# Kernel tuning notes

Measured on AMD Instinct MI355X. Metric: run time of the kernel, lower is better.

Reference implementation:

```python
import jax, jax.numpy as jnp
import numpy as np

NS = 100000; NT = 100000; M = 512; D = 256; DL = 128; H = 4; C = 256; K = 64
ITERS = 50; POS_MARGIN = 0.1


def conv1(w, b, x):
    # 1x1 Conv1d: x (B, Cin, N), w (Cout, Cin)
    return jnp.einsum('oi,bin->bon', w, x) + b[None, :, None]


def attn_block(p, x, src):
    # attentional propagation: MHA message + MLP([x, msg]) (residual added by caller)
    wq, bq, wk, bk, wv, bv, wm, bm, w1, b1, w2, b2 = p
    B, Dm, N = x.shape
    Dh = Dm // H
    Nm = src.shape[2]
    q = conv1(wq, bq, x).reshape(B, H, Dh, N)
    k = conv1(wk, bk, src).reshape(B, H, Dh, Nm)
    v = conv1(wv, bv, src).reshape(B, H, Dh, Nm)
    a = jax.nn.softmax(jnp.einsum('bhdn,bhdm->bhnm', q, k) * (1.0 / np.sqrt(Dh)), axis=-1)
    msg = jnp.einsum('bhnm,bhdm->bhdn', a, v).reshape(B, Dm, N)
    msg = conv1(wm, bm, msg)
    h = jax.nn.relu(conv1(w1, b1, jnp.concatenate([x, msg], axis=1)))
    return conv1(w2, b2, h)


def nn_id(points, nodes):
    # 1-NN node id per point; points (N,3), nodes (M,3)
    d = (jnp.sum(points * points, 1, keepdims=True) - 2.0 * points @ nodes.T
         + jnp.sum(nodes * nodes, 1)[None, :])
    return jnp.argmin(d, axis=1)


def build_patches(pcd_id, m, k):
    # grouping_wrapper: first k point indices assigned to each node, -1 padded
    n = pcd_id.shape[0]
    order = jnp.argsort(pcd_id)  # stable
    sid = pcd_id[order]
    starts = jnp.searchsorted(sid, jnp.arange(m))
    rank = jnp.arange(n) - starts[sid]
    patch = jnp.full((m, k), -1, jnp.int32)
    patch = patch.at[sid, rank].set(order.astype(jnp.int32), mode='drop')  # rank>=k dropped
    mask = (patch < 0).astype(jnp.float32)
    return jnp.where(patch < 0, 0, patch), mask


def log_optimal_transport(scores, alpha, iters):
    b, m, n = scores.shape
    bins0 = jnp.full((b, m, 1), alpha)
    bins1 = jnp.full((b, 1, n), alpha)
    corner = jnp.full((b, 1, 1), alpha)
    Z = jnp.concatenate([jnp.concatenate([scores, bins0], 2),
                         jnp.concatenate([bins1, corner], 2)], 1)
    norm = -np.log(m + n)
    log_mu = jnp.concatenate([jnp.full((m,), norm, jnp.float32), jnp.array([np.log(n) + norm], jnp.float32)])
    log_nu = jnp.concatenate([jnp.full((n,), norm, jnp.float32), jnp.array([np.log(m) + norm], jnp.float32)])
    log_mu = jnp.broadcast_to(log_mu, (b, m + 1))
    log_nu = jnp.broadcast_to(log_nu, (b, n + 1))

    def body(carry, _):
        u, v = carry
        u = log_mu - jax.nn.logsumexp(Z + v[:, None, :], axis=2)
        v = log_nu - jax.nn.logsumexp(Z + u[:, :, None], axis=1)
        return (u, v), None

    (u, v), _ = jax.lax.scan(body, (jnp.zeros((b, m + 1)), jnp.zeros((b, n + 1))), None, length=iters)
    return Z + u[:, :, None] + v[:, None, :] - norm


def rpmnet_sinkhorn(log_alpha, bins0, bins1, iters):
    b = log_alpha.shape[0]
    corner = jnp.zeros((b, 1, 1), log_alpha.dtype)
    la = jnp.concatenate([jnp.concatenate([log_alpha, bins0], 2),
                          jnp.concatenate([bins1, corner], 2)], 1)

    def body(la, _):
        row = la - jax.nn.logsumexp(la, axis=2, keepdims=True)
        la = jnp.concatenate([row[:, :-1, :], la[:, -1:, :]], axis=1)  # normalize all rows but slack
        col = la - jax.nn.logsumexp(la, axis=1, keepdims=True)
        la = jnp.concatenate([col[:, :, :-1], la[:, :, -1:]], axis=2)  # normalize all cols but slack
        return la, None

    la, _ = jax.lax.scan(body, la, None, length=iters)
    return la


def _forward(src_pcd_c, tgt_pcd_c, src_node_c, tgt_node_c, src_feats_c, tgt_feats_c,
             src_final_f, tgt_final_f, rot, trans, src_pcd_raw, tgt_pcd_raw,
             c_wq, c_bq, c_wk, c_bk, c_wv, c_bv, c_wm, c_bm, c_w1, c_b1, c_w2, c_b2,
             l_wq, l_bq, l_wk, l_bk, l_wv, l_bv, l_wm, l_bm, l_w1, l_b1, l_w2, l_b2,
             fp_w, fp_b, lfp_w, lfp_b, bin_score, node_corr):
    # KNN assignment + patch grouping (irregular gather/scatter)
    src_patch, src_mask = build_patches(nn_id(src_pcd_c, src_node_c), M, K)
    tgt_patch, tgt_mask = build_patches(nn_id(tgt_pcd_c, tgt_node_c), M, K)
    # coarse attention stack (self, cross, self) with residuals
    cp = lambda i: (c_wq[i], c_bq[i], c_wk[i], c_bk[i], c_wv[i], c_bv[i], c_wm[i], c_bm[i],
                    c_w1[i], c_b1[i], c_w2[i], c_b2[i])
    sf, tf = src_feats_c, tgt_feats_c
    sf = sf + attn_block(cp(0), sf, sf); tf = tf + attn_block(cp(0), tf, tf)
    sf = sf + attn_block(cp(1), sf, tf); tf = tf + attn_block(cp(1), tf, sf)  # sequential, like torch
    sf = sf + attn_block(cp(2), sf, sf); tf = tf + attn_block(cp(2), tf, tf)
    sf = conv1(fp_w, fp_b, sf); tf = conv1(fp_w, fp_b, tf)
    scores = jnp.einsum('bdn,bdm->bnm', sf, tf) / np.sqrt(D)
    scores = log_optimal_transport(scores, bin_score, ITERS)
    # correspondence-driven patch gather
    sn = node_corr[:, 0]; tn = node_corr[:, 1]
    src_sel = src_patch[sn].reshape(-1)
    tgt_sel = tgt_patch[tn].reshape(-1)
    smask = src_mask[sn]; tmask = tgt_mask[tn]  # (C,K)
    # GT local scores (training path)
    src_raw_t = (rot @ src_pcd_raw.T + trans).T
    sc = src_raw_t[src_sel].reshape(C, K, 3)
    tc = tgt_pcd_raw[tgt_sel].reshape(C, K, 3)
    d2 = jnp.maximum(jnp.sum(sc * sc, -1)[:, :, None] + jnp.sum(tc * tc, -1)[:, None, :]
                     - 2.0 * jnp.einsum('cnd,cmd->cnm', sc, tc), 0.0)
    gt = (jnp.sqrt(d2) < POS_MARGIN).astype(jnp.float32)
    row = jnp.maximum(1.0 - jnp.sum(gt, -1), 0.0)[:, :, None]
    col = jnp.maximum(1.0 - jnp.sum(gt, -2), 0.0)[:, None, :]
    col = jnp.concatenate([col, jnp.zeros((C, 1, 1), jnp.float32)], -1)
    gt = jnp.concatenate([jnp.concatenate([gt, row], -1), col], -2)  # (C,K+1,K+1)
    gt = gt.at[:, :-1, :].multiply(1.0 - smask[:, :, None])
    gt = gt.at[:, :, :-1].multiply(1.0 - tmask[:, None, :])
    # local patch features + attention stack
    spf = src_final_f[src_sel].reshape(C, K, DL).transpose(0, 2, 1)  # (C,DL,K)
    tpf = tgt_final_f[tgt_sel].reshape(C, K, DL).transpose(0, 2, 1)
    lp = lambda i: (l_wq[i], l_bq[i], l_wk[i], l_bk[i], l_wv[i], l_bv[i], l_wm[i], l_bm[i],
                    l_w1[i], l_b1[i], l_w2[i], l_b2[i])
    spf = spf + attn_block(lp(0), spf, spf); tpf = tpf + attn_block(lp(0), tpf, tpf)
    spf = spf + attn_block(lp(1), spf, tpf); tpf = tpf + attn_block(lp(1), tpf, spf)
    spf = spf + attn_block(lp(2), spf, spf); tpf = tpf + attn_block(lp(2), tpf, tpf)
    spf = conv1(lfp_w, lfp_b, spf); tpf = conv1(lfp_w, lfp_b, tpf)
    ls = jnp.einsum('bdn,bdm->bnm', spf, tpf) / np.sqrt(DL)
    ls = jnp.where(smask[:, :, None] > 0, -1e6, ls)
    ls = jnp.where(tmask[:, None, :] > 0, -1e6, ls)
    ls = rpmnet_sinkhorn(ls, jnp.zeros((C, K, 1), jnp.float32), jnp.zeros((C, 1, K), jnp.float32), ITERS)
    return scores, ls, gt


def setup_inputs() -> dict:
    key = jax.random.key(0)
    ks = jax.random.split(key, 48)

    def rn(i, shape, scale):
        return jax.random.normal(ks[i], shape, jnp.float32) * scale

    inp = {}
    inp['src_pcd_c'] = jax.random.uniform(ks[0], (NS, 3), jnp.float32)
    inp['tgt_pcd_c'] = jax.random.uniform(ks[1], (NT, 3), jnp.float32)
    inp['src_node_c'] = jax.random.uniform(ks[2], (M, 3), jnp.float32)
    inp['tgt_node_c'] = jax.random.uniform(ks[3], (M, 3), jnp.float32)
    inp['src_feats_c'] = rn(4, (1, D, M), 1.0)
    inp['tgt_feats_c'] = rn(5, (1, D, M), 1.0)
    inp['src_final_f'] = rn(6, (NS, DL), 1.0)
    inp['tgt_final_f'] = rn(7, (NT, DL), 1.0)
    inp['rot'] = jnp.eye(3, dtype=jnp.float32)
    inp['trans'] = jnp.zeros((3, 1), jnp.float32)
    inp['src_pcd_raw'] = jax.random.uniform(ks[8], (NS, 3), jnp.float32)
    inp['tgt_pcd_raw'] = jax.random.uniform(ks[9], (NT, 3), jnp.float32)
    inp['node_corr'] = jax.random.randint(ks[10], (C, 2), 0, M)
    i = 11
    for pre, d in (('c_', D), ('l_', DL)):
        for nm in ('wq', 'wk', 'wv', 'wm'):
            inp[pre + nm] = rn(i, (3, d, d), 1.0 / np.sqrt(d)); i += 1
            inp[pre + 'b' + nm[1]] = jnp.zeros((3, d), jnp.float32)
        inp[pre + 'w1'] = rn(i, (3, 2 * d, 2 * d), 1.0 / np.sqrt(2 * d)); i += 1
        inp[pre + 'b1'] = jnp.zeros((3, 2 * d), jnp.float32)
        inp[pre + 'w2'] = rn(i, (3, d, 2 * d), 1.0 / np.sqrt(2 * d)); i += 1
        inp[pre + 'b2'] = jnp.zeros((3, d), jnp.float32)
    inp['fp_w'] = rn(i, (D, D), 1.0 / np.sqrt(D)); i += 1
    inp['fp_b'] = jnp.zeros((D,), jnp.float32)
    inp['lfp_w'] = rn(i, (DL, DL), 1.0 / np.sqrt(DL)); i += 1
    inp['lfp_b'] = jnp.zeros((DL,), jnp.float32)
    inp['bin_score'] = jnp.ones((), jnp.float32)
    return inp


def reference(src_pcd_c, tgt_pcd_c, src_node_c, tgt_node_c, src_feats_c, tgt_feats_c,
              src_final_f, tgt_final_f, rot, trans, src_pcd_raw, tgt_pcd_raw,
              c_wq, c_bq, c_wk, c_bk, c_wv, c_bv, c_wm, c_bm, c_w1, c_b1, c_w2, c_b2,
              l_wq, l_bq, l_wk, l_bk, l_wv, l_bv, l_wm, l_bm, l_w1, l_b1, l_w2, l_b2,
              fp_w, fp_b, lfp_w, lfp_b, bin_score, node_corr):
    return _forward(src_pcd_c, tgt_pcd_c, src_node_c, tgt_node_c, src_feats_c, tgt_feats_c,
                    src_final_f, tgt_final_f, rot, trans, src_pcd_raw, tgt_pcd_raw,
                    c_wq, c_bq, c_wk, c_bk, c_wv, c_bv, c_wm, c_bm, c_w1, c_b1, c_w2, c_b2,
                    l_wq, l_bq, l_wk, l_bk, l_wv, l_bv, l_wm, l_bm, l_w1, l_b1, l_w2, l_b2,
                    fp_w, fp_b, lfp_w, lfp_b, bin_score, node_corr)
```

## Files before the change

kernel.cpp:

```cpp
#include <hip/hip_runtime.h>
#include <math.h>

static constexpr int NODES = 512;
static constexpr int CC    = 256;
static constexpr int KP    = 64;
static constexpr int ZDIM  = 513;
static constexpr int TPNB  = 16;
static constexpr int TPROWS = 33;

typedef unsigned short u16;
typedef short bf16x8 __attribute__((ext_vector_type(8)));
typedef float f32x4 __attribute__((ext_vector_type(4)));

__device__ __forceinline__ u16 f2b(float f){
  unsigned u = __float_as_uint(f);
  unsigned r = (u + 0x7FFF + ((u >> 16) & 1)) >> 16;
  return (u16)r;
}
__device__ __forceinline__ float b2f(u16 h){ return __uint_as_float(((unsigned)h) << 16); }
__device__ __forceinline__ f32x4 mfma16(bf16x8 a, bf16x8 b, f32x4 c){
  return __builtin_amdgcn_mfma_f32_16x16x32_bf16(a, b, c, 0, 0, 0);
}
__device__ __forceinline__ void astore(float* p, float v){
  __hip_atomic_store(p, v, __ATOMIC_RELAXED, __HIP_MEMORY_SCOPE_AGENT);
// ... 151 lines not shown
  __syncthreads();
  if (i >= n) return;
  int m = lid[t];
  int r = hist[(long)bb*NODES + m];
  for (int q = 0; q < t; ++q) r += (lid[q] == m) ? 1 : 0;
  if (r < KP) patch[m*KP + r] = i;
}

__global__ __launch_bounds__(256) void coarse_qkv(
    const u16* __restrict__ cf, int cross, int side0,
    const u16* __restrict__ Wq, const u16* __restrict__ Wk, const u16* __restrict__ Wv,
    const float* __restrict__ bq, const float* __restrict__ bk, const float* __restrict__ bv,
    u16* __restrict__ qb, u16* __restrict__ kb, u16* __restrict__ vtb)
{
  int z = blockIdx.x;
  int side = side0 + z/24, rem = z%24, proj = rem >> 3, slice = rem & 7;
  const u16* x = cf + (long)side*131072;
  const u16* s = cross ? cf + (long)(1-side)*131072 : x;
  const u16* in = (proj == 0) ? x : s;
  const u16* W  = (proj==0)?Wq:(proj==1)?Wk:Wv;
  const float* bi = (proj==0)?bq:(proj==1)?bk:bv;
  int n0 = slice << 6;
  int wv_ = threadIdx.x >> 6, L = threadIdx.x & 63, lr = L & 15, lk = L >> 4;
  const u16* inb = in + (long)(n0 + lr)*256 + 8*lk;
  for (int oi = 0; oi < 4; ++oi){
    int o0 = (wv_*4 + oi) << 4;
    const u16* wrow = W + (long)(o0 + lr)*256 + 8*lk;
    f32x4 acc[4] = {};
#pragma unroll
    for (int ks = 0; ks < 8; ++ks){
      bf16x8 b = *(const bf16x8*)(wrow + ks*32);
#pragma unroll
      for (int a = 0; a < 4; ++a){
        bf16x8 av = *(const bf16x8*)(inb + a*16*256 + ks*32);
        acc[a] = mfma16(av, b, acc[a]);
      }
    }
    int col = o0 + lr;
    float bvv = bi[col];
    if (proj < 2){
      u16* o = (proj==0 ? qb : kb) + ((long)side*512 + n0)*256 + col;
#pragma unroll
      for (int a = 0; a < 4; ++a)
#pragma unroll
        for (int q_ = 0; q_ < 4; ++q_)
          o[(long)(a*16 + lk*4 + q_)*256] = f2b(acc[a][q_] + bvv);
    } else {
      u16* o = vtb + ((long)side*256 + col)*512 + n0;
#pragma unroll
      for (int a = 0; a < 4; ++a)
#pragma unroll
        for (int q_ = 0; q_ < 4; ++q_)
          o[a*16 + lk*4 + q_] = f2b(acc[a][q_] + bvv);
    }
  }
}

__global__ __launch_bounds__(256) void coarse_attn(
    const u16* __restrict__ qb, const u16* __restrict__ kb,
    const u16* __restrict__ vtb, u16* __restrict__ msgb, int side0)
{
  __shared__ u16 P[64][512];
  __shared__ float rmx[64][4], rsm[64][4];
  int z = blockIdx.x;
  int side = side0 + (z >> 5); int rem = z & 31;
  int head = rem >> 3, qs = rem & 7;
  int wv_ = threadIdx.x >> 6, L = threadIdx.x & 63, lr = L & 15, lk = L >> 4;
  const u16* q = qb + ((long)side*512 + qs*64)*256 + head*64;
  const u16* k = kb + (long)side*512*256 + head*64;
  const u16* vt = vtb + ((long)side*256 + head*64)*512;

  bf16x8 af[4][2];
#pragma unroll
  for (int a = 0; a < 4; ++a)
#pragma unroll
    for (int ks = 0; ks < 2; ++ks)
      af[a][ks] = *(const bf16x8*)(q + (long)(a*16 + lr)*256 + ks*32 + 8*lk);

  f32x4 sc[4][8] = {};
  for (int b = 0; b < 8; ++b){
    const u16* krow = k + (long)(wv_*128 + b*16 + lr)*256 + 8*lk;
#pragma unroll
    for (int ks = 0; ks < 2; ++ks){
      bf16x8 bf = *(const bf16x8*)(krow + ks*32);
#pragma unroll
      for (int a = 0; a < 4; ++a)
        sc[a][b] = mfma16(af[a][ks], bf, sc[a][b]);
    }
  }
  const float SC = 0.125f;
#pragma unroll
  for (int a = 0; a < 4; ++a)
#pragma unroll
    for (int q_ = 0; q_ < 4; ++q_){
      float m = sc[a][0][q_];
#pragma unroll
      for (int b = 1; b < 8; ++b) m = fmaxf(m, sc[a][b][q_]);
      m = fmaxf(m, __shfl_xor(m, 1)); m = fmaxf(m, __shfl_xor(m, 2));
      m = fmaxf(m, __shfl_xor(m, 4)); m = fmaxf(m, __shfl_xor(m, 8));
      if (lr == 0) rmx[a*16 + lk*4 + q_][wv_] = m;
    }
  __syncthreads();
#pragma unroll
  for (int a = 0; a < 4; ++a)
#pragma unroll
    for (int q_ = 0; q_ < 4; ++q_){
      int row = a*16 + lk*4 + q_;
      float m = fmaxf(fmaxf(rmx[row][0], rmx[row][1]), fmaxf(rmx[row][2], rmx[row][3]));
      float s = 0.f;
#pragma unroll
      for (int b = 0; b < 8; ++b){
        float e = __expf((sc[a][b][q_] - m)*SC);
        sc[a][b][q_] = e; s += e;
      }
      s += __shfl_xor(s,1); s += __shfl_xor(s,2); s += __shfl_xor(s,4); s += __shfl_xor(s,8);
      if (lr == 0) rsm[row][wv_] = s;
    }
  __syncthreads();
#pragma unroll
  for (int a = 0; a < 4; ++a)
#pragma unroll
    for (int q_ = 0; q_ < 4; ++q_){
      int row = a*16 + lk*4 + q_;
      float inv = 1.f / (rsm[row][0]+rsm[row][1]+rsm[row][2]+rsm[row][3]);
#pragma unroll
      for (int b = 0; b < 8; ++b)
        P[row][wv_*128 + b*16 + lr] = f2b(sc[a][b][q_] * inv);
    }
  __syncthreads();
  f32x4 mv[4] = {};
  for (int ks = 0; ks < 16; ++ks){
    bf16x8 bf = *(const bf16x8*)(vt + (long)(wv_*16 + lr)*512 + ks*32 + 8*lk);
#pragma unroll
    for (int a = 0; a < 4; ++a){
      bf16x8 av = *(const bf16x8*)(&P[a*16 + lr][ks*32 + 8*lk]);
      mv[a] = mfma16(av, bf, mv[a]);
    }
  }
  u16* o = msgb + ((long)side*512 + qs*64)*256 + head*64 + wv_*16 + lr;
#pragma unroll
  for (int a = 0; a < 4; ++a)
#pragma unroll
    for (int q_ = 0; q_ < 4; ++q_)
      o[(long)(a*16 + lk*4 + q_)*256] = f2b(mv[a][q_]);
}

__global__ __launch_bounds__(512) void coarse_ffn(
    const u16* __restrict__ msgb, u16* __restrict__ cf, float* __restrict__ cff,
    const u16* __restrict__ Wm, const float* __restrict__ bm,
    const u16* __restrict__ W1, const float* __restrict__ b1,
    const u16* __restrict__ W2, const float* __restrict__ b2, int side0)
{
  __shared__ u16 m2[64*256];
  __shared__ u16 h1[64*512];
  int z = blockIdx.x;
  int side = side0 + (z >> 3), slice = z & 7;
  int wv_ = threadIdx.x >> 6, L = threadIdx.x & 63, lr = L & 15, lk = L >> 4;
  const u16* msg = msgb + ((long)side*512 + slice*64)*256;
  u16* x = cf + ((long)side*512 + slice*64)*256;
  float* xf = cff + ((long)side*512 + slice*64)*256;
  for (int oi = 0; oi < 2; ++oi){
    int o0 = (wv_*2 + oi) << 4;
    f32x4 acc[4] = {};
    const u16* wrow = Wm + (long)(o0+lr)*256 + 8*lk;
#pragma unroll
    for (int ks = 0; ks < 8; ++ks){
      bf16x8 b = *(const bf16x8*)(wrow + ks*32);
#pragma unroll
      for (int a = 0; a < 4; ++a){
        bf16x8 av = *(const bf16x8*)(msg + (long)(a*16+lr)*256 + ks*32 + 8*lk);
        acc[a] = mfma16(av, b, acc[a]);
      }
    }
    int col = o0 + lr; float bb = bm[col];
#pragma unroll
    for (int a = 0; a < 4; ++a)
#pragma unroll
      for (int q_ = 0; q_ < 4; ++q_)
        m2[(a*16+lk*4+q_)*256 + col] = f2b(acc[a][q_] + bb);
  }
  __syncthreads();
  for (int oi = 0; oi < 4; ++oi){
    int o0 = (wv_*4 + oi) << 4;
    f32x4 acc[4] = {};
    const u16* wrow = W1 + (long)(o0+lr)*512 + 8*lk;
#pragma unroll
    for (int ks = 0; ks < 16; ++ks){
      int kk = ks*32;
      bf16x8 b = *(const bf16x8*)(wrow + kk);
#pragma unroll
      for (int a = 0; a < 4; ++a){
        bf16x8 av;
        if (kk < 256) av = *(const bf16x8*)(x + (long)(a*16+lr)*256 + kk + 8*lk);
        else          av = *(const bf16x8*)(&m2[(a*16+lr)*256 + kk - 256 + 8*lk]);
        acc[a] = mfma16(av, b, acc[a]);
      }
    }
    int col = o0 + lr; float bb = b1[col];
#pragma unroll
    for (int a = 0; a < 4; ++a)
#pragma unroll
      for (int q_ = 0; q_ < 4; ++q_)
        h1[(a*16+lk*4+q_)*512 + col] = f2b(fmaxf(acc[a][q_] + bb, 0.f));
  }
  __syncthreads();
  for (int oi = 0; oi < 2; ++oi){
    int o0 = (wv_*2 + oi) << 4;
    f32x4 acc[4] = {};
    const u16* wrow = W2 + (long)(o0+lr)*512 + 8*lk;
#pragma unroll
    for (int ks = 0; ks < 16; ++ks){
      bf16x8 b = *(const bf16x8*)(wrow + ks*32);
#pragma unroll
      for (int a = 0; a < 4; ++a){
        bf16x8 av = *(const bf16x8*)(&h1[(a*16+lr)*512 + ks*32 + 8*lk]);
        acc[a] = mfma16(av, b, acc[a]);
      }
    }
    int col = o0 + lr; float bb = b2[col];
#pragma unroll
    for (int a = 0; a < 4; ++a)
#pragma unroll
      for (int q_ = 0; q_ < 4; ++q_){
        long idx = (long)(a*16+lk*4+q_)*256 + col;
        float v = acc[a][q_] + bb + xf[idx];
        xf[idx] = v;
        x[idx] = f2b(v);
      }
  }
}

__global__ __launch_bounds__(256) void coarse_proj(
    const u16* __restrict__ cf, const u16* __restrict__ W,
    const float* __restrict__ bias, u16* __restrict__ out)
{
  int z = blockIdx.x;
  int side = z >> 3, slice = z & 7;
  const u16* in = cf + (long)side*131072;
  u16* o = out + (long)side*131072;
  int n0 = slice << 6;
  int wv_ = threadIdx.x >> 6, L = threadIdx.x & 63, lr = L & 15, lk = L >> 4;
  const u16* inb = in + (long)(n0 + lr)*256 + 8*lk;
  for (int oi = 0; oi < 4; ++oi){
    int o0 = (wv_*4 + oi) << 4;
    const u16* wrow = W + (long)(o0 + lr)*256 + 8*lk;
    f32x4 acc[4] = {};
#pragma unroll
    for (int ks = 0; ks < 8; ++ks){
      bf16x8 b = *(const bf16x8*)(wrow + ks*32);
#pragma unroll
      for (int a = 0; a < 4; ++a){
        bf16x8 av = *(const bf16x8*)(inb + a*16*256 + ks*32);
        acc[a] = mfma16(av, b, acc[a]);
      }
    }
    int col = o0 + lr; float bb = bias[col];
#pragma unroll
    for (int a = 0; a < 4; ++a)
#pragma unroll
      for (int q_ = 0; q_ < 4; ++q_)
        o[(long)(n0 + a*16 + lk*4 + q_)*256 + col] = f2b(acc[a][q_] + bb);
  }
}

__global__ __launch_bounds__(256) void coarse_scores(
    const u16* __restrict__ sfp, const u16* __restrict__ tfp, float* __restrict__ Z)
{
  int n0 = blockIdx.y << 6, m0 = blockIdx.x << 6;
  int wv_ = threadIdx.x >> 6, L = threadIdx.x & 63, lr = L & 15, lk = L >> 4;
  f32x4 acc[4] = {};
  const u16* arow = sfp + (long)(n0 + lr)*256 + 8*lk;
  const u16* brow = tfp + (long)(m0 + wv_*16 + lr)*256 + 8*lk;
#pragma unroll
// ... 149 lines not shown
    for (int j = lane; j < 513; j += 64) orow[j] = zr[j] + uu + M[j] + outadd;
  }
}

__device__ void layerapp(
    u16* __restrict__ x, const u16* __restrict__ s, u16* __restrict__ pool,
    const u16* __restrict__ Wq, const u16* __restrict__ Wk,
    const u16* __restrict__ Wv, const u16* __restrict__ Wm,
    const u16* __restrict__ W1, const u16* __restrict__ W2,
    const float* __restrict__ bq, const float* __restrict__ bk,
    const float* __restrict__ bv, const float* __restrict__ bm,
    const float* __restrict__ b1, const float* __restrict__ b2)
{
  int tid = threadIdx.x;
  int wv8 = tid >> 6, L = tid & 63, lr = L & 15, lk = L >> 4;
  u16* qS = pool; u16* kS = pool + 8192; u16* vT = pool + 16384; u16* msgS = pool + 24576;

#pragma unroll
  for (int proj = 0; proj < 3; ++proj){
    const u16* in = proj ? s : x;
    const u16* W = proj==0?Wq:proj==1?Wk:Wv;
    const float* bi = proj==0?bq:proj==1?bk:bv;
    int o0 = wv8 << 4;
    f32x4 acc[4] = {};
    const u16* wrow = W + (long)(o0+lr)*128 + 8*lk;
    const u16* inr = in + (long)lr*128 + 8*lk;
#pragma unroll
    for (int ks = 0; ks < 4; ++ks){
      bf16x8 b = *(const bf16x8*)(wrow + ks*32);
#pragma unroll
      for (int a = 0; a < 4; ++a){
        bf16x8 av = *(const bf16x8*)(inr + a*16*128 + ks*32);
        acc[a] = mfma16(av, b, acc[a]);
      }
    }
    int col = o0 + lr; float bb = bi[col];
    if (proj < 2){
      u16* dst = (proj==0 ? qS : kS);
#pragma unroll
      for (int a = 0; a < 4; ++a)
#pragma unroll
        for (int q_ = 0; q_ < 4; ++q_)
          dst[(a*16 + lk*4 + q_)*128 + col] = f2b(acc[a][q_] + bb);
    } else {
#pragma unroll
      for (int a = 0; a < 4; ++a)
#pragma unroll
        for (int q_ = 0; q_ < 4; ++q_)
          vT[col*64 + a*16 + lk*4 + q_] = f2b(acc[a][q_] + bb);
    }
  }
  __syncthreads();
  int h = wv8 >> 1, half = wv8 & 1;
  bf16x8 qf[2], kf[4];
#pragma unroll
  for (int ai = 0; ai < 2; ++ai){
    int a = half*2 + ai;
    qf[ai] = *(const bf16x8*)(&qS[(a*16+lr)*128 + h*32 + 8*lk]);
  }
#pragma unroll
  for (int b = 0; b < 4; ++b)
    kf[b] = *(const bf16x8*)(&kS[(b*16+lr)*128 + h*32 + 8*lk]);
  f32x4 sc[2][4] = {};
#pragma unroll
  for (int b = 0; b < 4; ++b)
#pragma unroll
    for (int ai = 0; ai < 2; ++ai)
      sc[ai][b] = mfma16(qf[ai], kf[b], sc[ai][b]);
  const float SCs = 0.17677669529663687f;
  float invs[2][4];
#pragma unroll
  for (int ai = 0; ai < 2; ++ai)
#pragma unroll
    for (int q_ = 0; q_ < 4; ++q_){
      float m = sc[ai][0][q_];
#pragma unroll
      for (int b = 1; b < 4; ++b) m = fmaxf(m, sc[ai][b][q_]);
// ... 2 lines not shown
      float ss = 0.f;
#pragma unroll
      for (int b = 0; b < 4; ++b){
        float e = __expf((sc[ai][b][q_] - m)*SCs);
        sc[ai][b][q_] = e; ss += e;
      }
      ss += __shfl_xor(ss,1); ss += __shfl_xor(ss,2); ss += __shfl_xor(ss,4); ss += __shfl_xor(ss,8);
      invs[ai][q_] = 1.f/ss;
    }
  __syncthreads();
  u16* P = pool + h*4096;
#pragma unroll
  for (int ai = 0; ai < 2; ++ai){
    int a = half*2 + ai;
#pragma unroll
    for (int q_ = 0; q_ < 4; ++q_)
#pragma unroll
      for (int b = 0; b < 4; ++b)
        P[(a*16 + lk*4 + q_)*64 + b*16 + lr] = f2b(sc[ai][b][q_] * invs[ai][q_]);
  }
  f32x4 mv[2][2] = {};
#pragma unroll
  for (int ks = 0; ks < 2; ++ks)
#pragma unroll
    for (int bt = 0; bt < 2; ++bt){
      bf16x8 bf = *(const bf16x8*)(&vT[(h*32 + bt*16 + lr)*64 + ks*32 + 8*lk]);
#pragma unroll
      for (int ai = 0; ai < 2; ++ai){
        int a = half*2 + ai;
        bf16x8 av = *(const bf16x8*)(&P[(a*16+lr)*64 + ks*32 + 8*lk]);
        mv[ai][bt] = mfma16(av, bf, mv[ai][bt]);
      }
    }
#pragma unroll
  for (int ai = 0; ai < 2; ++ai){
    int a = half*2 + ai;
#pragma unroll
    for (int bt = 0; bt < 2; ++bt)
#pragma unroll
      for (int q_ = 0; q_ < 4; ++q_)
        msgS[(a*16 + lk*4 + q_)*128 + h*32 + bt*16 + lr] = f2b(mv[ai][bt][q_]);
  }
  __syncthreads();
  u16* m2 = pool;
  {
    int o0 = wv8 << 4;
    f32x4 acc[4] = {};
    const u16* wrow = Wm + (long)(o0+lr)*128 + 8*lk;
#pragma unroll
    for (int ks = 0; ks < 4; ++ks){
      bf16x8 b = *(const bf16x8*)(wrow + ks*32);
#pragma unroll
      for (int a = 0; a < 4; ++a){
        bf16x8 av = *(const bf16x8*)(&msgS[(a*16+lr)*128 + ks*32 + 8*lk]);
        acc[a] = mfma16(av, b, acc[a]);
      }
    }
    int col = o0+lr; float bb = bm[col];
#pragma unroll
    for (int a = 0; a < 4; ++a)
#pragma unroll
      for (int q_ = 0; q_ < 4; ++q_)
        m2[(a*16+lk*4+q_)*128 + col] = f2b(acc[a][q_] + bb);
  }
  __syncthreads();
  u16* h1 = pool + 8192;
#pragma unroll
  for (int oi = 0; oi < 2; ++oi){
    int o0 = (wv8*2 + oi) << 4;
    f32x4 acc[4] = {};
    const u16* wrow = W1 + (long)(o0+lr)*256 + 8*lk;
#pragma unroll
    for (int ks = 0; ks < 8; ++ks){
      int kk = ks*32;
      bf16x8 b = *(const bf16x8*)(wrow + kk);
#pragma unroll
      for (int a = 0; a < 4; ++a){
        bf16x8 av;
        if (kk < 128) av = *(const bf16x8*)(x + (long)(a*16+lr)*128 + kk + 8*lk);
        else          av = *(const bf16x8*)(&m2[(a*16+lr)*128 + kk - 128 + 8*lk]);
        acc[a] = mfma16(av, b, acc[a]);
      }
    }
    int col = o0+lr; float bb = b1[col];
#pragma unroll
    for (int a = 0; a < 4; ++a)
#pragma unroll
      for (int q_ = 0; q_ < 4; ++q_)
        h1[(a*16+lk*4+q_)*256 + col] = f2b(fmaxf(acc[a][q_] + bb, 0.f));
  }
  __syncthreads();
  {
    int o0 = wv8 << 4;
    f32x4 acc[4] = {};
    const u16* wrow = W2 + (long)(o0+lr)*256 + 8*lk;
#pragma unroll
    for (int ks = 0; ks < 8; ++ks){
      bf16x8 b = *(const bf16x8*)(wrow + ks*32);
#pragma unroll
      for (int a = 0; a < 4; ++a){
        bf16x8 av = *(const bf16x8*)(&h1[(a*16+lr)*256 + ks*32 + 8*lk]);
        acc[a] = mfma16(av, b, acc[a]);
      }
    }
    int col = o0+lr; float bb = b2[col];
#pragma unroll
    for (int a = 0; a < 4; ++a)
#pragma unroll
      for (int q_ = 0; q_ < 4; ++q_){
        int ri = (a*16+lk*4+q_)*128 + col;
        x[ri] = f2b(acc[a][q_] + bb + b2f(x[ri]));
      }
  }
  __syncthreads();
}

__device__ void local_role(char* arena, int c,
    const float* __restrict__ Fs, const float* __restrict__ Ft,
    const int* __restrict__ patch_s, const int* __restrict__ patch_t,
    const int* __restrict__ corr,
    const int* __restrict__ cnt_s, const int* __restrict__ cnt_t,
    const u16* WlQ, const u16* WlK, const u16* WlV, const u16* WlM,
    const u16* Wl1, const u16* Wl2, const u16* Wlfp,
    const float* lbq, const float* lbk, const float* lbv, const float* lbm,
    const float* lb1, const float* lb2, const float* lfpB,
    float* __restrict__ out_ls)
{
  u16* X    = (u16*)arena;
  u16* pool = (u16*)(arena + 32768);
  float* LA = (float*)(arena + 98304);
  float* ET = (float*)(arena + 115712);
  float* uvec = (float*)(arena + 133120);
  float* vvec = (float*)(arena + 133440);
  float* u0s  = (float*)(arena + 133760);
  float* Ul   = (float*)(arena + 134080);
  float* Vl   = (float*)(arena + 134400);
  int* sel    = (int*)(arena + 134720);
  int tid = threadIdx.x;
  int wv8 = tid >> 6, L = tid & 63, lr = L & 15, lk = L >> 4;

  if (tid < 128){
    int side = tid >> 6, n = tid & 63;
    int node = corr[c*2 + side];
    sel[tid] = (side ? patch_t : patch_s)[node*KP + n];
  }
  __syncthreads();
  for (int e = tid; e < 16384; e += 512){
    int side = e >> 13, r = e & 8191, n = r >> 7, d = r & 127;
    const float* F = side ? Ft : Fs;
    X[e] = f2b(F[(long)sel[side*64 + n]*128 + d]);
  }
  __syncthreads();

  for (int l = 0; l < 3; ++l){
// ... 18 lines not shown
    const u16* wrow = Wlfp + (long)(o0+lr)*128 + 8*lk;
    const u16* inr = in + (long)lr*128 + 8*lk;
#pragma unroll
    for (int ks = 0; ks < 4; ++ks){
      bf16x8 b = *(const bf16x8*)(wrow + ks*32);
#pragma unroll
      for (int a = 0; a < 4; ++a){
        bf16x8 av = *(const bf16x8*)(inr + a*16*128 + ks*32);
        acc[a] = mfma16(av, b, acc[a]);
      }
    }
    int col = o0 + lr; float bb = lfpB[col];
#pragma unroll
    for (int a = 0; a < 4; ++a)
#pragma unroll
      for (int q_ = 0; q_ < 4; ++q_)
        dst[(a*16 + lk*4 + q_)*128 + col] = f2b(acc[a][q_] + bb);
  }
  __syncthreads();

  int cs = cnt_s[corr[c*2]], ct = cnt_t[corr[c*2+1]];
  for (int t_ = wv8; t_ < 16; t_ += 8){
    int mt = t_ >> 2, nt = t_ & 3;
    f32x4 acc = {};
    const u16* arow = sp + (mt*16 + lr)*128 + 8*lk;
    const u16* brow = tp + (nt*16 + lr)*128 + 8*lk;
#pragma unroll
    for (int ks = 0; ks < 4; ++ks){
      bf16x8 a = *(const bf16x8*)(arow + ks*32);
      bf16x8 b = *(const bf16x8*)(brow + ks*32);
      acc = mfma16(a, b, acc);
    }
    const float SCS = 0.08838834764831845f;
#pragma unroll
    for (int q_ = 0; q_ < 4; ++q_){
      int row = mt*16 + lk*4 + q_;
      int col = nt*16 + lr;
      float v = acc[q_] * SCS;
      if (row >= cs || col >= ct) v = -1000000.0f;
      LA[row*66 + col] = v;
    }
  }
  if (tid < 65){ LA[64*66 + tid] = 0.f; LA[tid*66 + 64] = 0.f; uvec[tid] = 1.f; vvec[tid] = 1.f; }
  __syncthreads();

// ... 126 lines not shown
    const float* lbq, const float* lbk, const float* lbv, const float* lbm,
    const float* lb1, const float* lb2, const float* lfpB,
    float* out_ls,
    const float* sraw, const float* traw, const float* rot, const float* trans,
    float* out_gt)
{
  __shared__ __align__(16) char arena[ARENA];
  int b = blockIdx.x;
  if (b < 128){
    if ((b & 7) == 0)
      transport_role(arena, b >> 3, Z, Zt, Rr, Cc, UU, VV, out0, outadd);
    return;
  }
  b -= 128;
  if (b < CC)
    gt_role(arena, b, sraw, traw, rot, trans,
            patch_s, patch_t, corr, cnt_s, cnt_t, out_gt);
  else
    local_role(arena, b - CC, Fs, Ft, patch_s, patch_t, corr, cnt_s, cnt_t,
               WlQ, WlK, WlV, WlM, Wl1, Wl2, Wlfp,
               lbq, lbk, lbv, lbm, lb1, lb2, lfpB, out_ls);
}

extern "C" void kernel_launch(void* const* d_in, const int* in_sizes, int n_in,
                              void* d_out, int out_size, void* d_ws, size_t ws_size,
                              hipStream_t stream)
{
  const float* src_pcd_c  = (const float*)d_in[0];
  const float* tgt_pcd_c  = (const float*)d_in[1];
  const float* src_node_c = (const float*)d_in[2];
  const float* tgt_node_c = (const float*)d_in[3];
  const float* src_feats  = (const float*)d_in[4];
  const float* tgt_feats  = (const float*)d_in[5];
  const float* src_final  = (const float*)d_in[6];
  const float* tgt_final  = (const float*)d_in[7];
  const float* rot        = (const float*)d_in[8];
// ... 82 lines not shown
      tgt_pcd_c, NT, tgt_node_c, id_t, hist_t, nbs, nbnn,
      src_feats, tgt_feats, cf, cff);
  scan_kernel2<<<256, 256, 0, stream>>>(hist_s, nbs, cnt_s, hist_t, nbt, cnt_t);
  rank_kernel<<<nbs + nbt, 256, 0, stream>>>(
      id_s, NS, hist_s, patch_s, id_t, NT, hist_t, patch_t, nbs);

  int crossL[3] = {0, 1, 0};
  for (int l = 0; l < 3; ++l){
    u16* wq = WcQ + (size_t)l*65536; u16* wk = WcK + (size_t)l*65536;
    u16* wv = WcV + (size_t)l*65536; u16* wm = WcM + (size_t)l*65536;
    u16* w1 = Wc1 + (size_t)l*262144; u16* w2 = Wc2 + (size_t)l*131072;
    const float* bq = c_bq + (size_t)l*256; const float* bk = c_bk + (size_t)l*256;
    const float* bv = c_bv + (size_t)l*256; const float* bm = c_bm + (size_t)l*256;
    const float* b1 = c_b1 + (size_t)l*512; const float* b2 = c_b2 + (size_t)l*256;
    if (!crossL[l]){
      coarse_qkv<<<48, 256, 0, stream>>>(cf, 0, 0, wq, wk, wv, bq, bk, bv, qb, kb, vtb);
      coarse_attn<<<64, 256, 0, stream>>>(qb, kb, vtb, msgb, 0);
      coarse_ffn<<<16, 512, 0, stream>>>(msgb, cf, cff, wm, bm, w1, b1, w2, b2, 0);
    } else {
      for (int sd = 0; sd < 2; ++sd){
        coarse_qkv<<<24, 256, 0, stream>>>(cf, 1, sd, wq, wk, wv, bq, bk, bv, qb, kb, vtb);
        coarse_attn<<<32, 256, 0, stream>>>(qb, kb, vtb, msgb, sd);
        coarse_ffn<<<8, 512, 0, stream>>>(msgb, cf, cff, wm, bm, w1, b1, w2, b2, sd);
      }
    }
  }
  coarse_proj<<<16, 256, 0, stream>>>(cf, Wfp, fp_b, sfpb);
  coarse_scores<<<dim3(8,8), 256, 0, stream>>>(sfpb, sfpb + 131072, Zx);
  fill_border<<<3, 256, 0, stream>>>(Zx, bin_score);
  transpose_k<<<dim3(17,17), 256, 0, stream>>>(Zx, Zt, ZDIM);

  mega<<<128 + CC + CC, 512, 0, stream>>>(
      Zx, Zt, Rr, Cc, UU, VV, out0, logf(1024.0f),
      src_final, tgt_final, patch_s, patch_t, node_corr, cnt_s, cnt_t,
      WlQ, WlK, WlV, WlM, Wl1, Wl2, Wlfp,
      l_bq, l_bk, l_bv, l_bm, l_b1, l_b2, lfp_b,
      out_ls,
      src_raw, tgt_raw, rot, trans, out_gt);

  (void)n_in; (void)out_size; (void)ws_size;
}
```

Measured before the change: 971.7 us.

## Shrink coarse-layer tiles for more blocks, swizzle LDS layouts, reorder mega roles

The coarse QKV, attention, projection and FFN kernels now use smaller row tiles (32 or 16 rows instead of 64), so each launch has two to four times as many blocks and the GPU's compute units are better filled. Shared-memory tiles in the coarse and local attention paths use an XOR swizzle, plus a padded vT stride, to avoid LDS bank conflicts on MFMA operand loads. The mega kernel now puts local_role blocks before gt_role blocks so the heavier work is scheduled earlier. In exchange, weight rows are reloaded from global memory by more blocks, and each block does less MFMA work per weight load.

```diff
diff --git a/kernel.cpp b/kernel.cpp
--- a/kernel.cpp
+++ b/kernel.cpp
@@ -189,24 +189,24 @@
     u16* __restrict__ qb, u16* __restrict__ kb, u16* __restrict__ vtb)
 {
   int z = blockIdx.x;
-  int side = side0 + z/24, rem = z%24, proj = rem >> 3, slice = rem & 7;
+  int side = side0 + z/48, rem = z%48, proj = rem >> 4, slice = rem & 15;
   const u16* x = cf + (long)side*131072;
   const u16* s = cross ? cf + (long)(1-side)*131072 : x;
   const u16* in = (proj == 0) ? x : s;
   const u16* W  = (proj==0)?Wq:(proj==1)?Wk:Wv;
   const float* bi = (proj==0)?bq:(proj==1)?bk:bv;
-  int n0 = slice << 6;
+  int n0 = slice << 5;
   int wv_ = threadIdx.x >> 6, L = threadIdx.x & 63, lr = L & 15, lk = L >> 4;
   const u16* inb = in + (long)(n0 + lr)*256 + 8*lk;
   for (int oi = 0; oi < 4; ++oi){
     int o0 = (wv_*4 + oi) << 4;
     const u16* wrow = W + (long)(o0 + lr)*256 + 8*lk;
-    f32x4 acc[4] = {};
+    f32x4 acc[2] = {};
 #pragma unroll
     for (int ks = 0; ks < 8; ++ks){
       bf16x8 b = *(const bf16x8*)(wrow + ks*32);
 #pragma unroll
-      for (int a = 0; a < 4; ++a){
+      for (int a = 0; a < 2; ++a){
         bf16x8 av = *(const bf16x8*)(inb + a*16*256 + ks*32);
         acc[a] = mfma16(av, b, acc[a]);
       }
@@ -216,14 +216,14 @@
     if (proj < 2){
       u16* o = (proj==0 ? qb : kb) + ((long)side*512 + n0)*256 + col;
 #pragma unroll
-      for (int a = 0; a < 4; ++a)
+      for (int a = 0; a < 2; ++a)
 #pragma unroll
         for (int q_ = 0; q_ < 4; ++q_)
           o[(long)(a*16 + lk*4 + q_)*256] = f2b(acc[a][q_] + bvv);
     } else {
       u16* o = vtb + ((long)side*256 + col)*512 + n0;
 #pragma unroll
-      for (int a = 0; a < 4; ++a)
+      for (int a = 0; a < 2; ++a)
 #pragma unroll
         for (int q_ = 0; q_ < 4; ++q_)
           o[a*16 + lk*4 + q_] = f2b(acc[a][q_] + bvv);
@@ -235,37 +235,37 @@
     const u16* __restrict__ qb, const u16* __restrict__ kb,
     const u16* __restrict__ vtb, u16* __restrict__ msgb, int side0)
 {
-  __shared__ u16 P[64][512];
-  __shared__ float rmx[64][4], rsm[64][4];
+  __shared__ u16 P[32*512];
+  __shared__ float rmx[32][4], rsm[32][4];
   int z = blockIdx.x;
-  int side = side0 + (z >> 5); int rem = z & 31;
-  int head = rem >> 3, qs = rem & 7;
+  int side = side0 + (z >> 6); int rem = z & 63;
+  int head = rem >> 4, qs = rem & 15;
   int wv_ = threadIdx.x >> 6, L = threadIdx.x & 63, lr = L & 15, lk = L >> 4;
-  const u16* q = qb + ((long)side*512 + qs*64)*256 + head*64;
+  const u16* q = qb + ((long)side*512 + qs*32)*256 + head*64;
   const u16* k = kb + (long)side*512*256 + head*64;
   const u16* vt = vtb + ((long)side*256 + head*64)*512;
 
-  bf16x8 af[4][2];
-#pragma unroll
-  for (int a = 0; a < 4; ++a)
+  bf16x8 af[2][2];
+#pragma unroll
+  for (int a = 0; a < 2; ++a)
 #pragma unroll
     for (int ks = 0; ks < 2; ++ks)
       af[a][ks] = *(const bf16x8*)(q + (long)(a*16 + lr)*256 + ks*32 + 8*lk);
 
-  f32x4 sc[4][8] = {};
+  f32x4 sc[2][8] = {};
   for (int b = 0; b < 8; ++b){
     const u16* krow = k + (long)(wv_*128 + b*16 + lr)*256 + 8*lk;
 #pragma unroll
     for (int ks = 0; ks < 2; ++ks){
       bf16x8 bf = *(const bf16x8*)(krow + ks*32);
 #pragma unroll
-      for (int a = 0; a < 4; ++a)
+      for (int a = 0; a < 2; ++a)
         sc[a][b] = mfma16(af[a][ks], bf, sc[a][b]);
     }
   }
   const float SC = 0.125f;
 #pragma unroll
-  for (int a = 0; a < 4; ++a)
+  for (int a = 0; a < 2; ++a)
 #pragma unroll
     for (int q_ = 0; q_ < 4; ++q_){
       float m = sc[a][0][q_];
@@ -277,7 +277,7 @@
     }
   __syncthreads();
 #pragma unroll
-  for (int a = 0; a < 4; ++a)
+  for (int a = 0; a < 2; ++a)
 #pragma unroll
     for (int q_ = 0; q_ < 4; ++q_){
       int row = a*16 + lk*4 + q_;
@@ -293,115 +293,104 @@
     }
   __syncthreads();
 #pragma unroll
-  for (int a = 0; a < 4; ++a)
+  for (int a = 0; a < 2; ++a)
 #pragma unroll
     for (int q_ = 0; q_ < 4; ++q_){
       int row = a*16 + lk*4 + q_;
       float inv = 1.f / (rsm[row][0]+rsm[row][1]+rsm[row][2]+rsm[row][3]);
 #pragma unroll
       for (int b = 0; b < 8; ++b)
-        P[row][wv_*128 + b*16 + lr] = f2b(sc[a][b][q_] * inv);
-    }
-  __syncthreads();
-  f32x4 mv[4] = {};
+        P[row*512 + ((wv_*128 + b*16 + lr) ^ ((row&7)<<3))] = f2b(sc[a][b][q_] * inv);
+    }
+  __syncthreads();
+  f32x4 mv[2] = {};
   for (int ks = 0; ks < 16; ++ks){
     bf16x8 bf = *(const bf16x8*)(vt + (long)(wv_*16 + lr)*512 + ks*32 + 8*lk);
 #pragma unroll
-    for (int a = 0; a < 4; ++a){
-      bf16x8 av = *(const bf16x8*)(&P[a*16 + lr][ks*32 + 8*lk]);
+    for (int a = 0; a < 2; ++a){
+      bf16x8 av = *(const bf16x8*)(&P[(a*16 + lr)*512 + ((ks*32 + 8*lk) ^ ((lr&7)<<3))]);
       mv[a] = mfma16(av, bf, mv[a]);
     }
   }
-  u16* o = msgb + ((long)side*512 + qs*64)*256 + head*64 + wv_*16 + lr;
-#pragma unroll
-  for (int a = 0; a < 4; ++a)
+  u16* o = msgb + ((long)side*512 + qs*32)*256 + head*64 + wv_*16 + lr;
+#pragma unroll
+  for (int a = 0; a < 2; ++a)
 #pragma unroll
     for (int q_ = 0; q_ < 4; ++q_)
       o[(long)(a*16 + lk*4 + q_)*256] = f2b(mv[a][q_]);
 }
 
-__global__ __launch_bounds__(512) void coarse_ffn(
+__global__ __launch_bounds__(256) void coarse_ffn(
     const u16* __restrict__ msgb, u16* __restrict__ cf, float* __restrict__ cff,
     const u16* __restrict__ Wm, const float* __restrict__ bm,
     const u16* __restrict__ W1, const float* __restrict__ b1,
     const u16* __restrict__ W2, const float* __restrict__ b2, int side0)
 {
-  __shared__ u16 m2[64*256];
-  __shared__ u16 h1[64*512];
+  __shared__ u16 m2[16*256];
+  __shared__ u16 h1[16*512];
   int z = blockIdx.x;
-  int side = side0 + (z >> 3), slice = z & 7;
+  int side = side0 + (z >> 5), slice = z & 31;
   int wv_ = threadIdx.x >> 6, L = threadIdx.x & 63, lr = L & 15, lk = L >> 4;
-  const u16* msg = msgb + ((long)side*512 + slice*64)*256;
-  u16* x = cf + ((long)side*512 + slice*64)*256;
-  float* xf = cff + ((long)side*512 + slice*64)*256;
-  for (int oi = 0; oi < 2; ++oi){
-    int o0 = (wv_*2 + oi) << 4;
-    f32x4 acc[4] = {};
+  const u16* msg = msgb + ((long)side*512 + slice*16)*256;
+  u16* x = cf + ((long)side*512 + slice*16)*256;
+  float* xf = cff + ((long)side*512 + slice*16)*256;
+  for (int oi = 0; oi < 4; ++oi){
+    int o0 = (wv_*4 + oi) << 4;
+    f32x4 acc = {};
     const u16* wrow = Wm + (long)(o0+lr)*256 + 8*lk;
 #pragma unroll
     for (int ks = 0; ks < 8; ++ks){
       bf16x8 b = *(const bf16x8*)(wrow + ks*32);
-#pragma unroll
-      for (int a = 0; a < 4; ++a){
-        bf16x8 av = *(const bf16x8*)(msg + (long)(a*16+lr)*256 + ks*32 + 8*lk);
-        acc[a] = mfma16(av, b, acc[a]);
-      }
+      bf16x8 av = *(const bf16x8*)(msg + (long)lr*256 + ks*32 + 8*lk);
+      acc = mfma16(av, b, acc);
     }
     int col = o0 + lr; float bb = bm[col];
 #pragma unroll
-    for (int a = 0; a < 4; ++a)
-#pragma unroll
-      for (int q_ = 0; q_ < 4; ++q_)
-        m2[(a*16+lk*4+q_)*256 + col] = f2b(acc[a][q_] + bb);
-  }
-  __syncthreads();
-  for (int oi = 0; oi < 4; ++oi){
-    int o0 = (wv_*4 + oi) << 4;
-    f32x4 acc[4] = {};
+    for (int q_ = 0; q_ < 4; ++q_){
+      int row = lk*4 + q_;
+      m2[row*256 + (col ^ ((row&7)<<3))] = f2b(acc[q_] + bb);
+    }
+  }
+  __syncthreads();
+  for (int oi = 0; oi < 8; ++oi){
+    int o0 = (wv_*8 + oi) << 4;
+    f32x4 acc = {};
     const u16* wrow = W1 + (long)(o0+lr)*512 + 8*lk;
 #pragma unroll
     for (int ks = 0; ks < 16; ++ks){
       int kk = ks*32;
       bf16x8 b = *(const bf16x8*)(wrow + kk);
-#pragma unroll
-      for (int a = 0; a < 4; ++a){
-        bf16x8 av;
-        if (kk < 256) av = *(const bf16x8*)(x + (long)(a*16+lr)*256 + kk + 8*lk);
-        else          av = *(const bf16x8*)(&m2[(a*16+lr)*256 + kk - 256 + 8*lk]);
-        acc[a] = mfma16(av, b, acc[a]);
-      }
+      bf16x8 av;
+      if (kk < 256) av = *(const bf16x8*)(x + (long)lr*256 + kk + 8*lk);
+      else          av = *(const bf16x8*)(&m2[lr*256 + ((kk - 256 + 8*lk) ^ ((lr&7)<<3))]);
+      acc = mfma16(av, b, acc);
     }
     int col = o0 + lr; float bb = b1[col];
 #pragma unroll
-    for (int a = 0; a < 4; ++a)
-#pragma unroll
-      for (int q_ = 0; q_ < 4; ++q_)
-        h1[(a*16+lk*4+q_)*512 + col] = f2b(fmaxf(acc[a][q_] + bb, 0.f));
-  }
-  __syncthreads();
-  for (int oi = 0; oi < 2; ++oi){
-    int o0 = (wv_*2 + oi) << 4;
-    f32x4 acc[4] = {};
+    for (int q_ = 0; q_ < 4; ++q_){
+      int row = lk*4 + q_;
+      h1[row*512 + (col ^ ((row&7)<<3))] = f2b(fmaxf(acc[q_] + bb, 0.f));
+    }
+  }
+  __syncthreads();
+  for (int oi = 0; oi < 4; ++oi){
+    int o0 = (wv_*4 + oi) << 4;
+    f32x4 acc = {};
     const u16* wrow = W2 + (long)(o0+lr)*512 + 8*lk;
 #pragma unroll
     for (int ks = 0; ks < 16; ++ks){
       bf16x8 b = *(const bf16x8*)(wrow + ks*32);
-#pragma unroll
-      for (int a = 0; a < 4; ++a){
-        bf16x8 av = *(const bf16x8*)(&h1[(a*16+lr)*512 + ks*32 + 8*lk]);
-        acc[a] = mfma16(av, b, acc[a]);
-      }
+      bf16x8 av = *(const bf16x8*)(&h1[lr*512 + ((ks*32 + 8*lk) ^ ((lr&7)<<3))]);
+      acc = mfma16(av, b, acc);
     }
     int col = o0 + lr; float bb = b2[col];
 #pragma unroll
-    for (int a = 0; a < 4; ++a)
-#pragma unroll
-      for (int q_ = 0; q_ < 4; ++q_){
-        long idx = (long)(a*16+lk*4+q_)*256 + col;
-        float v = acc[a][q_] + bb + xf[idx];
-        xf[idx] = v;
-        x[idx] = f2b(v);
-      }
+    for (int q_ = 0; q_ < 4; ++q_){
+      long idx = (long)(lk*4+q_)*256 + col;
+      float v = acc[q_] + bb + xf[idx];
+      xf[idx] = v;
+      x[idx] = f2b(v);
+    }
   }
 }
 
@@ -410,28 +399,28 @@
     const float* __restrict__ bias, u16* __restrict__ out)
 {
   int z = blockIdx.x;
-  int side = z >> 3, slice = z & 7;
+  int side = z >> 4, slice = z & 15;
   const u16* in = cf + (long)side*131072;
   u16* o = out + (long)side*131072;
-  int n0 = slice << 6;
+  int n0 = slice << 5;
   int wv_ = threadIdx.x >> 6, L = threadIdx.x & 63, lr = L & 15, lk = L >> 4;
   const u16* inb = in + (long)(n0 + lr)*256 + 8*lk;
   for (int oi = 0; oi < 4; ++oi){
     int o0 = (wv_*4 + oi) << 4;
     const u16* wrow = W + (long)(o0 + lr)*256 + 8*lk;
-    f32x4 acc[4] = {};
+    f32x4 acc[2] = {};
 #pragma unroll
     for (int ks = 0; ks < 8; ++ks){
       bf16x8 b = *(const bf16x8*)(wrow + ks*32);
 #pragma unroll
-      for (int a = 0; a < 4; ++a){
+      for (int a = 0; a < 2; ++a){
         bf16x8 av = *(const bf16x8*)(inb + a*16*256 + ks*32);
         acc[a] = mfma16(av, b, acc[a]);
       }
     }
     int col = o0 + lr; float bb = bias[col];
 #pragma unroll
-    for (int a = 0; a < 4; ++a)
+    for (int a = 0; a < 2; ++a)
 #pragma unroll
       for (int q_ = 0; q_ < 4; ++q_)
         o[(long)(n0 + a*16 + lk*4 + q_)*256 + col] = f2b(acc[a][q_] + bb);
@@ -611,7 +600,8 @@
 {
   int tid = threadIdx.x;
   int wv8 = tid >> 6, L = tid & 63, lr = L & 15, lk = L >> 4;
-  u16* qS = pool; u16* kS = pool + 8192; u16* vT = pool + 16384; u16* msgS = pool + 24576;
+  u16* qS = pool; u16* kS = pool + 8192; u16* vT = pool + 16384; u16* msgS = pool + 24832;
+  int swr = (lr & 7) << 3;
 
 #pragma unroll
   for (int proj = 0; proj < 3; ++proj){
@@ -637,14 +627,16 @@
 #pragma unroll
       for (int a = 0; a < 4; ++a)
 #pragma unroll
+        for (int q_ = 0; q_ < 4; ++q_){
+          int row = a*16 + lk*4 + q_;
+          dst[row*128 + (col ^ ((row&7)<<3))] = f2b(acc[a][q_] + bb);
+        }
+    } else {
+#pragma unroll
+      for (int a = 0; a < 4; ++a)
+#pragma unroll
         for (int q_ = 0; q_ < 4; ++q_)
-          dst[(a*16 + lk*4 + q_)*128 + col] = f2b(acc[a][q_] + bb);
-    } else {
-#pragma unroll
-      for (int a = 0; a < 4; ++a)
-#pragma unroll
-        for (int q_ = 0; q_ < 4; ++q_)
-          vT[col*64 + a*16 + lk*4 + q_] = f2b(acc[a][q_] + bb);
+          vT[col*66 + a*16 + lk*4 + q_] = f2b(acc[a][q_] + bb);
     }
   }
   __syncthreads();
@@ -653,11 +645,11 @@
 #pragma unroll
   for (int ai = 0; ai < 2; ++ai){
     int a = half*2 + ai;
-    qf[ai] = *(const bf16x8*)(&qS[(a*16+lr)*128 + h*32 + 8*lk]);
+    qf[ai] = *(const bf16x8*)(&qS[(a*16+lr)*128 + ((h*32 + 8*lk) ^ swr)]);
   }
 #pragma unroll
   for (int b = 0; b < 4; ++b)
-    kf[b] = *(const bf16x8*)(&kS[(b*16+lr)*128 + h*32 + 8*lk]);
+    kf[b] = *(const bf16x8*)(&kS[(b*16+lr)*128 + ((h*32 + 8*lk) ^ swr)]);
   f32x4 sc[2][4] = {};
 #pragma unroll
   for (int b = 0; b < 4; ++b)
@@ -690,21 +682,23 @@
   for (int ai = 0; ai < 2; ++ai){
     int a = half*2 + ai;
 #pragma unroll
-    for (int q_ = 0; q_ < 4; ++q_)
+    for (int q_ = 0; q_ < 4; ++q_){
+      int row = a*16 + lk*4 + q_;
 #pragma unroll
       for (int b = 0; b < 4; ++b)
-        P[(a*16 + lk*4 + q_)*64 + b*16 + lr] = f2b(sc[ai][b][q_] * invs[ai][q_]);
+        P[row*64 + ((b*16 + lr) ^ ((row&7)<<3))] = f2b(sc[ai][b][q_] * invs[ai][q_]);
+    }
   }
   f32x4 mv[2][2] = {};
 #pragma unroll
   for (int ks = 0; ks < 2; ++ks)
 #pragma unroll
     for (int bt = 0; bt < 2; ++bt){
-      bf16x8 bf = *(const bf16x8*)(&vT[(h*32 + bt*16 + lr)*64 + ks*32 + 8*lk]);
+      bf16x8 bf = *(const bf16x8*)(&vT[(h*32 + bt*16 + lr)*66 + ks*32 + 8*lk]);
 #pragma unroll
       for (int ai = 0; ai < 2; ++ai){
         int a = half*2 + ai;
-        bf16x8 av = *(const bf16x8*)(&P[(a*16+lr)*64 + ks*32 + 8*lk]);
+        bf16x8 av = *(const bf16x8*)(&P[(a*16+lr)*64 + ((ks*32 + 8*lk) ^ swr)]);
         mv[ai][bt] = mfma16(av, bf, mv[ai][bt]);
       }
     }
@@ -714,8 +708,10 @@
 #pragma unroll
     for (int bt = 0; bt < 2; ++bt)
 #pragma unroll
-      for (int q_ = 0; q_ < 4; ++q_)
-        msgS[(a*16 + lk*4 + q_)*128 + h*32 + bt*16 + lr] = f2b(mv[ai][bt][q_]);
+      for (int q_ = 0; q_ < 4; ++q_){
+        int row = a*16 + lk*4 + q_;
+        msgS[row*128 + ((h*32 + bt*16 + lr) ^ ((row&7)<<3))] = f2b(mv[ai][bt][q_]);
+      }
   }
   __syncthreads();
   u16* m2 = pool;
@@ -728,7 +724,7 @@
       bf16x8 b = *(const bf16x8*)(wrow + ks*32);
 #pragma unroll
       for (int a = 0; a < 4; ++a){
-        bf16x8 av = *(const bf16x8*)(&msgS[(a*16+lr)*128 + ks*32 + 8*lk]);
+        bf16x8 av = *(const bf16x8*)(&msgS[(a*16+lr)*128 + ((ks*32 + 8*lk) ^ swr)]);
         acc[a] = mfma16(av, b, acc[a]);
       }
     }
@@ -736,8 +732,10 @@
 #pragma unroll
     for (int a = 0; a < 4; ++a)
 #pragma unroll
-      for (int q_ = 0; q_ < 4; ++q_)
-        m2[(a*16+lk*4+q_)*128 + col] = f2b(acc[a][q_] + bb);
+      for (int q_ = 0; q_ < 4; ++q_){
+        int row = a*16+lk*4+q_;
+        m2[row*128 + (col ^ ((row&7)<<3))] = f2b(acc[a][q_] + bb);
+      }
   }
   __syncthreads();
   u16* h1 = pool + 8192;
@@ -754,7 +752,7 @@
       for (int a = 0; a < 4; ++a){
         bf16x8 av;
         if (kk < 128) av = *(const bf16x8*)(x + (long)(a*16+lr)*128 + kk + 8*lk);
-        else          av = *(const bf16x8*)(&m2[(a*16+lr)*128 + kk - 128 + 8*lk]);
+        else          av = *(const bf16x8*)(&m2[(a*16+lr)*128 + ((kk - 128 + 8*lk) ^ swr)]);
         acc[a] = mfma16(av, b, acc[a]);
       }
     }
@@ -762,8 +760,10 @@
 #pragma unroll
     for (int a = 0; a < 4; ++a)
 #pragma unroll
-      for (int q_ = 0; q_ < 4; ++q_)
-        h1[(a*16+lk*4+q_)*256 + col] = f2b(fmaxf(acc[a][q_] + bb, 0.f));
+      for (int q_ = 0; q_ < 4; ++q_){
+        int row = a*16+lk*4+q_;
+        h1[row*256 + (col ^ ((row&7)<<3))] = f2b(fmaxf(acc[a][q_] + bb, 0.f));
+      }
   }
   __syncthreads();
   {
@@ -775,7 +775,7 @@
       bf16x8 b = *(const bf16x8*)(wrow + ks*32);
 #pragma unroll
       for (int a = 0; a < 4; ++a){
-        bf16x8 av = *(const bf16x8*)(&h1[(a*16+lr)*256 + ks*32 + 8*lk]);
+        bf16x8 av = *(const bf16x8*)(&h1[(a*16+lr)*256 + ((ks*32 + 8*lk) ^ swr)]);
         acc[a] = mfma16(av, b, acc[a]);
       }
     }
@@ -804,16 +804,17 @@
 {
   u16* X    = (u16*)arena;
   u16* pool = (u16*)(arena + 32768);
-  float* LA = (float*)(arena + 98304);
-  float* ET = (float*)(arena + 115712);
-  float* uvec = (float*)(arena + 133120);
-  float* vvec = (float*)(arena + 133440);
-  float* u0s  = (float*)(arena + 133760);
-  float* Ul   = (float*)(arena + 134080);
-  float* Vl   = (float*)(arena + 134400);
-  int* sel    = (int*)(arena + 134720);
+  float* LA = (float*)(arena + 98816);
+  float* ET = (float*)(arena + 115976);
+  float* uvec = (float*)(arena + 133136);
+  float* vvec = (float*)(arena + 133456);
+  float* u0s  = (float*)(arena + 133776);
+  float* Ul   = (float*)(arena + 134096);
+  float* Vl   = (float*)(arena + 134416);
+  int* sel    = (int*)(arena + 134736);
   int tid = threadIdx.x;
   int wv8 = tid >> 6, L = tid & 63, lr = L & 15, lk = L >> 4;
+  int swr = (lr & 7) << 3;
 
   if (tid < 128){
     int side = tid >> 6, n = tid & 63;
@@ -862,8 +863,10 @@
 #pragma unroll
     for (int a = 0; a < 4; ++a)
 #pragma unroll
-      for (int q_ = 0; q_ < 4; ++q_)
-        dst[(a*16 + lk*4 + q_)*128 + col] = f2b(acc[a][q_] + bb);
+      for (int q_ = 0; q_ < 4; ++q_){
+        int row = a*16 + lk*4 + q_;
+        dst[row*128 + (col ^ ((row&7)<<3))] = f2b(acc[a][q_] + bb);
+      }
   }
   __syncthreads();
 
@@ -871,12 +874,10 @@
   for (int t_ = wv8; t_ < 16; t_ += 8){
     int mt = t_ >> 2, nt = t_ & 3;
     f32x4 acc = {};
-    const u16* arow = sp + (mt*16 + lr)*128 + 8*lk;
-    const u16* brow = tp + (nt*16 + lr)*128 + 8*lk;
 #pragma unroll
     for (int ks = 0; ks < 4; ++ks){
-      bf16x8 a = *(const bf16x8*)(arow + ks*32);
-      bf16x8 b = *(const bf16x8*)(brow + ks*32);
+      bf16x8 a = *(const bf16x8*)(&sp[(mt*16 + lr)*128 + ((ks*32 + 8*lk) ^ swr)]);
+      bf16x8 b = *(const bf16x8*)(&tp[(nt*16 + lr)*128 + ((ks*32 + 8*lk) ^ swr)]);
       acc = mfma16(a, b, acc);
     }
     const float SCS = 0.08838834764831845f;
@@ -1033,12 +1034,12 @@
   }
   b -= 128;
   if (b < CC)
-    gt_role(arena, b, sraw, traw, rot, trans,
-            patch_s, patch_t, corr, cnt_s, cnt_t, out_gt);
-  else
-    local_role(arena, b - CC, Fs, Ft, patch_s, patch_t, corr, cnt_s, cnt_t,
+    local_role(arena, b, Fs, Ft, patch_s, patch_t, corr, cnt_s, cnt_t,
                WlQ, WlK, WlV, WlM, Wl1, Wl2, Wlfp,
                lbq, lbk, lbv, lbm, lb1, lb2, lfpB, out_ls);
+  else
+    gt_role(arena, b - CC, sraw, traw, rot, trans,
+            patch_s, patch_t, corr, cnt_s, cnt_t, out_gt);
 }
 
 extern "C" void kernel_launch(void* const* d_in, const int* in_sizes, int n_in,
@@ -1151,18 +1152,18 @@
     const float* bv = c_bv + (size_t)l*256; const float* bm = c_bm + (size_t)l*256;
     const float* b1 = c_b1 + (size_t)l*512; const float* b2 = c_b2 + (size_t)l*256;
     if (!crossL[l]){
-      coarse_qkv<<<48, 256, 0, stream>>>(cf, 0, 0, wq, wk, wv, bq, bk, bv, qb, kb, vtb);
-      coarse_attn<<<64, 256, 0, stream>>>(qb, kb, vtb, msgb, 0);
-      coarse_ffn<<<16, 512, 0, stream>>>(msgb, cf, cff, wm, bm, w1, b1, w2, b2, 0);
+      coarse_qkv<<<96, 256, 0, stream>>>(cf, 0, 0, wq, wk, wv, bq, bk, bv, qb, kb, vtb);
+      coarse_attn<<<128, 256, 0, stream>>>(qb, kb, vtb, msgb, 0);
+      coarse_ffn<<<64, 256, 0, stream>>>(msgb, cf, cff, wm, bm, w1, b1, w2, b2, 0);
     } else {
       for (int sd = 0; sd < 2; ++sd){
-        coarse_qkv<<<24, 256, 0, stream>>>(cf, 1, sd, wq, wk, wv, bq, bk, bv, qb, kb, vtb);
-        coarse_attn<<<32, 256, 0, stream>>>(qb, kb, vtb, msgb, sd);
-        coarse_ffn<<<8, 512, 0, stream>>>(msgb, cf, cff, wm, bm, w1, b1, w2, b2, sd);
-      }
-    }
-  }
-  coarse_proj<<<16, 256, 0, stream>>>(cf, Wfp, fp_b, sfpb);
+        coarse_qkv<<<48, 256, 0, stream>>>(cf, 1, sd, wq, wk, wv, bq, bk, bv, qb, kb, vtb);
+        coarse_attn<<<64, 256, 0, stream>>>(qb, kb, vtb, msgb, sd);
+        coarse_ffn<<<32, 256, 0, stream>>>(msgb, cf, cff, wm, bm, w1, b1, w2, b2, sd);
+      }
+    }
+  }
+  coarse_proj<<<32, 256, 0, stream>>>(cf, Wfp, fp_b, sfpb);
   coarse_scores<<<dim3(8,8), 256, 0, stream>>>(sfpb, sfpb + 131072, Zx);
   fill_border<<<3, 256, 0, stream>>>(Zx, bin_score);
   transpose_k<<<dim3(17,17), 256, 0, stream>>>(Zx, Zt, ZDIM);
```

New measurement: 844.2 us. -13.1%, faster.
